# Performance work log

Hardware: AMD Instinct MI355X
Metric: run time of the kernel (lower is better)

The kernel has to match this reference:

```python
import jax, jax.numpy as jnp
import numpy as np

TAU = 0.2          # rank_temperature
LAM = 8.0          # lambda_value
TOPO = 0.5         # topology_influence
LEN_C = 0.01       # edge_length_coeff
SP_C = 0.001       # edge_sparsity_coeff
B, M, D = 4096, 256, 256


def _pairwise_sq(a, b):
    # [Na, D] x [Nb, D] -> [Na, Nb] squared L2 distances
    sq = (jnp.sum(a * a, -1)[:, None] - 2.0 * (a @ b.T)
          + jnp.sum(b * b, -1)[None, :])
    return jnp.maximum(sq, 0.0)


def setup_inputs() -> dict:
    key = jax.random.key(0)
    k1, k2, k3 = jax.random.split(key, 3)
    data = jax.random.normal(k1, (B, D), dtype=jnp.float32)
    weights = jax.random.uniform(k2, (M, D), dtype=jnp.float32)
    # edge logits initialized near edge_init_logit (-2.0) with small noise
    edge_logits = -2.0 + 0.1 * jax.random.normal(k3, (M, M), dtype=jnp.float32)
    return {"data": data, "weights": weights, "edge_logits": edge_logits}


def reference(data, weights, edge_logits):
    m = weights.shape[0]
    eye = jnp.eye(m, dtype=data.dtype)

    # distances: [B, M], l2
    distances = jnp.sqrt(_pairwise_sq(data, weights))

    # soft rank: [B, M]; pairwise sigmoid with zeroed diagonal
    diff = (distances[:, :, None] - distances[:, None, :]) / TAU  # [B, M, M]
    prob_greater = jax.nn.sigmoid(diff) * (1.0 - eye)[None]
    soft_rank = 1.0 + jnp.sum(prob_greater, axis=-1)

    # exponential neighborhood weighting
    neighborhood = jnp.exp(-(soft_rank - 1.0) / LAM)

    # symmetric edge probabilities with zero diagonal
    logits = 0.5 * (edge_logits + edge_logits.T)
    edge_prob = jax.nn.sigmoid(logits) * (1.0 - eye)

    degree = jnp.sum(edge_prob, axis=1) / float(m - 1)
    neighborhood = neighborhood * (1.0 + TOPO * degree[None, :])

    data_term = jnp.mean(neighborhood * distances)

    proto_dist = _pairwise_sq(weights, weights)  # sq_l2
    weighted_len = jnp.sum(edge_prob * proto_dist) / (jnp.sum(edge_prob) + 1e-8)
    sparsity = jnp.mean(edge_prob)

    loss = data_term + LEN_C * weighted_len + SP_C * sparsity
    return loss
```

## Files before the change

### kernel.cpp

```cpp
#include <hip/hip_runtime.h>
#include <math.h>

#define B_N 4096
#define M_N 256
#define D_N 256
#define ROWS 4
#define GRID_MAIN (B_N / ROWS)
#define NSLOT 64
#define BLK_PER_SLOT (GRID_MAIN / NSLOT)

constexpr float TAU_   = 0.2f;
constexpr float LAM_   = 8.0f;
constexpr float TOPO_  = 0.5f;
constexpr float LEN_C_ = 0.01f;
constexpr float SP_C_  = 0.001f;
constexpr float LOG2E_ = 1.44269504088896340736f;
constexpr float KSC    = LOG2E_ / TAU_;
constexpr float KL     = LOG2E_ / LAM_;
constexpr float C0_    = 133.0f;


__device__ __forceinline__ float wave_reduce_sum(float v) {
#pragma unroll
  for (int off = 1; off < 64; off <<= 1) v += __shfl_xor(v, off, 64);
  return v;
}

__global__ __launch_bounds__(256) void k_prep(const float* __restrict__ w,
                                              const float* __restrict__ E,
                                              float* __restrict__ ws) {
  int tid = threadIdx.x;
  if (blockIdx.x < M_N) {
    float* wT = ws + 8192;
    int j = blockIdx.x, d = tid;
    float v = w[j * D_N + d];
    wT[d * M_N + j] = v;
    float s = wave_reduce_sum(v * v);
    __shared__ float red[4];
    if ((d & 63) == 0) red[d >> 6] = s;
    if (j == 0) {
      if (d < 16) ws[d] = 0.0f;
      if (d < NSLOT) {
        ws[2048 + 16 * d] = 0.0f;
        ((unsigned*)ws)[4096 + 16 * d] = 0u;
      }
    }
    __syncthreads();
    if (d == 0) ws[512 + j] = red[0] + red[1] + red[2] + red[3];
  } else {
    int j = blockIdx.x - M_N;
    int k = tid;
    __shared__ __align__(16) float swj[D_N];
    __shared__ float redp[4], redw[4];
    swj[k] = w[j * D_N + k];
    __syncthreads();

    float l = 0.5f * (E[j * M_N + k] + E[k * M_N + j]);
    float p = __builtin_amdgcn_rcpf(1.0f + __builtin_amdgcn_exp2f(-l * LOG2E_));
    if (k == j) p = 0.0f;

    float pd = 0.0f;
    const float4* wr = (const float4*)(w + (size_t)k * D_N);
    const float4* sw = (const float4*)swj;
#pragma unroll 8
    for (int i = 0; i < D_N / 4; i++) {
      float4 a = wr[i], b = sw[i];
      float dx = a.x - b.x, dy = a.y - b.y, dz = a.z - b.z, dw = a.w - b.w;
      pd += dx * dx + dy * dy + dz * dz + dw * dw;
    }

    float sp  = wave_reduce_sum(p);
    float spd = wave_reduce_sum(p * pd);
    if ((k & 63) == 0) { redp[k >> 6] = sp; redw[k >> 6] = spd; }
    __syncthreads();
    if (k == 0) {
      float tp = redp[0] + redp[1] + redp[2] + redp[3];
      float tw = redw[0] + redw[1] + redw[2] + redw[3];
      ws[16 + j]   = tp * (1.0f / (float)(M_N - 1));
      ws[1024 + j] = tp;
      ws[1280 + j] = tw;
    }
  }
}

__global__ __launch_bounds__(256) void k_main(const float* __restrict__ data,
                                              float* __restrict__ ws,
                                              float* __restrict__ out) {
  const float* wT     = ws + 8192;
  const float* wnorm  = ws + 512;
  const float* degree = ws + 16;
  float* S_slot  = ws + 2048;
  unsigned* cnt1 = (unsigned*)ws + 4096;
  unsigned* cnt2 = (unsigned*)ws + 4;

  __shared__ __align__(16) float ew[ROWS][M_N];
  __shared__ __align__(16) float ewp[ROWS][M_N];
  __shared__ float rednrm[ROWS][4];
  __shared__ float snrm[ROWS];
  __shared__ float redf[4], redp[4], redw[4];
  __shared__ int isLast;

  const int tid  = threadIdx.x;
  const int wv_  = tid >> 6;
  const int lane = tid & 63;
  const int b0   = blockIdx.x * ROWS;

#pragma unroll
  for (int r = 0; r < ROWS; r++) {
    float x = data[(size_t)(b0 + r) * D_N + tid];
    float s = wave_reduce_sum(x * x);
    if (lane == 0) rednrm[r][wv_] = s;
  }
  __syncthreads();
  if (tid < ROWS)
    snrm[tid] = rednrm[tid][0] + rednrm[tid][1] + rednrm[tid][2] + rednrm[tid][3];

  const float4* x0 = (const float4*)(data + (size_t)(b0 + 0) * D_N);
  const float4* x1 = (const float4*)(data + (size_t)(b0 + 1) * D_N);
  const float4* x2 = (const float4*)(data + (size_t)(b0 + 2) * D_N);
  const float4* x3 = (const float4*)(data + (size_t)(b0 + 3) * D_N);
  float a0 = 0.f, a1 = 0.f, a2 = 0.f, a3 = 0.f;
#pragma unroll 4
  for (int d4 = 0; d4 < D_N / 4; d4++) {
    float4 xa = x0[d4], xb = x1[d4], xc = x2[d4], xd = x3[d4];
    const float* p = wT + (size_t)(4 * d4) * M_N + tid;
    float w0 = p[0], w1 = p[M_N], w2 = p[2 * M_N], w3 = p[3 * M_N];
    a0 = fmaf(xa.x, w0, a0); a0 = fmaf(xa.y, w1, a0);
    a0 = fmaf(xa.z, w2, a0); a0 = fmaf(xa.w, w3, a0);
    a1 = fmaf(xb.x, w0, a1); a1 = fmaf(xb.y, w1, a1);
    a1 = fmaf(xb.z, w2, a1); a1 = fmaf(xb.w, w3, a1);
    a2 = fmaf(xc.x, w0, a2); a2 = fmaf(xc.y, w1, a2);
    a2 = fmaf(xc.z, w2, a2); a2 = fmaf(xc.w, w3, a2);
    a3 = fmaf(xd.x, w0, a3); a3 = fmaf(xd.y, w1, a3);
    a3 = fmaf(xd.z, w2, a3); a3 = fmaf(xd.w, w3, a3);
  }
  __syncthreads();

  float wn = wnorm[tid];
  float acc[ROWS] = {a0, a1, a2, a3};
  float dist[ROWS], iv[ROWS], iv2[ROWS];
#pragma unroll
  for (int r = 0; r < ROWS; r++) {
    float sq = snrm[r] - 2.0f * acc[r] + wn;
    dist[r] = sqrtf(fmaxf(sq, 0.0f));
    float sc = dist[r] * KSC;
    ew[r][tid] = __builtin_amdgcn_exp2f(sc - C0_);
    iv[r]      = __builtin_amdgcn_exp2f(C0_ - sc);
    iv2[r]     = iv[r] * iv[r];
  }
  __syncthreads();

#pragma unroll
  for (int h = 0; h < 2; h++) {
    int p  = tid + h * 256;
    int r  = p >> 7, idx = p & 127;
    float ea = ew[r][2 * idx], eb = ew[r][2 * idx + 1];
    ewp[r][2 * idx]     = ea + eb;
    ewp[r][2 * idx + 1] = ea * eb;
  }
  __syncthreads();

  float fj = 1.0f + TOPO_ * degree[tid];
  float tl = 0.0f;
#pragma unroll
  for (int r = 0; r < ROWS; r++) {
    float s = 0.0f;
    const float4* q4 = (const float4*)(&ewp[r][0]);
    float ivr = iv[r], iv2r = iv2[r];
#pragma unroll 8
    for (int k4 = 0; k4 < M_N / 4; k4++) {
      float4 q = q4[k4];
      float t1 = ivr * q.x;
      s = fmaf(t1 + 2.0f, __builtin_amdgcn_rcpf(fmaf(iv2r, q.y, t1 + 1.0f)), s);
      float t2 = ivr * q.z;
      s = fmaf(t2 + 2.0f, __builtin_amdgcn_rcpf(fmaf(iv2r, q.w, t2 + 1.0f)), s);
    }
    float nb = __builtin_amdgcn_exp2f((0.5f - s) * KL);
    tl = fmaf(nb * dist[r], fj, tl);
  }

  float bs = wave_reduce_sum(tl);
  if (lane == 0) redf[wv_] = bs;
  __syncthreads();
  if (tid == 0) {
    float tot = redf[0] + redf[1] + redf[2] + redf[3];
    int slot = (int)(blockIdx.x & (NSLOT - 1));
    float old = atomicAdd(&S_slot[16 * slot], tot);
    asm volatile("" : "+v"(old));
    int last = 0;
    unsigned t1 = atomicAdd(&cnt1[16 * slot], 1u);
    if (t1 == (unsigned)(BLK_PER_SLOT - 1)) {
      unsigned t2 = atomicAdd(cnt2, 1u);
      last = (t2 == (unsigned)(NSLOT - 1)) ? 1 : 0;
    }
    isLast = last;
  }
  __syncthreads();

  if (isLast) {
    float p  = ws[1024 + tid];
    float wd = ws[1280 + tid];
    float rp = wave_reduce_sum(p);
    float rw = wave_reduce_sum(wd);
    if (lane == 0) { redp[wv_] = rp; redw[wv_] = rw; }
    float sd = 0.0f;
    if (wv_ == 0) {
      float v = atomicAdd(&S_slot[16 * lane], 0.0f);
      sd = wave_reduce_sum(v);
    }
    __syncthreads();
    if (tid == 0) {
      float Sp   = redp[0] + redp[1] + redp[2] + redp[3];
      float Swpd = redw[0] + redw[1] + redw[2] + redw[3];
      float data_term = sd * (1.0f / ((float)B_N * (float)M_N));
      float wl = Swpd / (Sp + 1e-8f);
      float sparsity = Sp * (1.0f / ((float)M_N * (float)M_N));
      out[0] = data_term + LEN_C_ * wl + SP_C_ * sparsity;
    }
  }
}

extern "C" void kernel_launch(void* const* d_in, const int* in_sizes, int n_in,
                              void* d_out, int out_size, void* d_ws, size_t ws_size,
                              hipStream_t stream) {
  const float* data = (const float*)d_in[0];
  const float* w    = (const float*)d_in[1];
  const float* E    = (const float*)d_in[2];
  float* ws = (float*)d_ws;

  k_prep<<<2 * M_N, 256, 0, stream>>>(w, E, ws);
  k_main<<<GRID_MAIN, 256, 0, stream>>>(data, ws, (float*)d_out);
}
```

Before: 102.2 us.

## Overlap soft-rank of rows 0-1 with distance matmul of rows 2-3

Splits the per-block work into two halves: the dot products for the first two data rows are computed first, and then their soft-rank pairwise loop is interleaved with the weight loads and FMAs for the remaining two rows. The aim is to hide global/L2 latency of the wT and data loads behind the transcendental-heavy rank computation instead of running the two phases back to back. In exchange it adds extra barriers and a second ewp build pass, raises register pressure from the 16-entry weight buffer, and re-reads wT per row pair.

New measurement: 114.5 us. +12.1%, slower.

```diff
diff --git a/kernel.cpp b/kernel.cpp
--- a/kernel.cpp
+++ b/kernel.cpp
@@ -24,6 +24,12 @@
 #pragma unroll
   for (int off = 1; off < 64; off <<= 1) v += __shfl_xor(v, off, 64);
   return v;
+}
+
+__device__ __forceinline__ void rank_pair(float iv, float iv2, float es,
+                                          float ep, float& s) {
+  float t = iv * es;
+  s = fmaf(t + 2.0f, __builtin_amdgcn_rcpf(fmaf(iv2, ep, t + 1.0f)), s);
 }
 
 __global__ __launch_bounds__(256) void k_prep(const float* __restrict__ w,
@@ -119,29 +125,26 @@
   const float4* x1 = (const float4*)(data + (size_t)(b0 + 1) * D_N);
   const float4* x2 = (const float4*)(data + (size_t)(b0 + 2) * D_N);
   const float4* x3 = (const float4*)(data + (size_t)(b0 + 3) * D_N);
-  float a0 = 0.f, a1 = 0.f, a2 = 0.f, a3 = 0.f;
-#pragma unroll 4
+
+  float a0 = 0.f, a1 = 0.f;
+#pragma unroll 8
   for (int d4 = 0; d4 < D_N / 4; d4++) {
-    float4 xa = x0[d4], xb = x1[d4], xc = x2[d4], xd = x3[d4];
     const float* p = wT + (size_t)(4 * d4) * M_N + tid;
     float w0 = p[0], w1 = p[M_N], w2 = p[2 * M_N], w3 = p[3 * M_N];
+    float4 xa = x0[d4], xb = x1[d4];
     a0 = fmaf(xa.x, w0, a0); a0 = fmaf(xa.y, w1, a0);
     a0 = fmaf(xa.z, w2, a0); a0 = fmaf(xa.w, w3, a0);
     a1 = fmaf(xb.x, w0, a1); a1 = fmaf(xb.y, w1, a1);
     a1 = fmaf(xb.z, w2, a1); a1 = fmaf(xb.w, w3, a1);
-    a2 = fmaf(xc.x, w0, a2); a2 = fmaf(xc.y, w1, a2);
-    a2 = fmaf(xc.z, w2, a2); a2 = fmaf(xc.w, w3, a2);
-    a3 = fmaf(xd.x, w0, a3); a3 = fmaf(xd.y, w1, a3);
-    a3 = fmaf(xd.z, w2, a3); a3 = fmaf(xd.w, w3, a3);
   }
   __syncthreads();
 
   float wn = wnorm[tid];
-  float acc[ROWS] = {a0, a1, a2, a3};
   float dist[ROWS], iv[ROWS], iv2[ROWS];
 #pragma unroll
-  for (int r = 0; r < ROWS; r++) {
-    float sq = snrm[r] - 2.0f * acc[r] + wn;
+  for (int r = 0; r < 2; r++) {
+    float a = (r == 0) ? a0 : a1;
+    float sq = snrm[r] - 2.0f * a + wn;
     dist[r] = sqrtf(fmaxf(sq, 0.0f));
     float sc = dist[r] * KSC;
     ew[r][tid] = __builtin_amdgcn_exp2f(sc - C0_);
@@ -150,32 +153,89 @@
   }
   __syncthreads();
 
-#pragma unroll
-  for (int h = 0; h < 2; h++) {
-    int p  = tid + h * 256;
-    int r  = p >> 7, idx = p & 127;
+  {
+    int r = tid >> 7, idx = tid & 127;
     float ea = ew[r][2 * idx], eb = ew[r][2 * idx + 1];
     ewp[r][2 * idx]     = ea + eb;
     ewp[r][2 * idx + 1] = ea * eb;
   }
   __syncthreads();
 
+  float a2 = 0.f, a3 = 0.f;
+  float s0 = 0.f, s1 = 0.f;
+  const float4* q0 = (const float4*)(&ewp[0][0]);
+  const float4* q1 = (const float4*)(&ewp[1][0]);
+  float iv0 = iv[0], iv20 = iv2[0], iv1 = iv[1], iv21 = iv2[1];
+#pragma unroll 2
+  for (int g = 0; g < 16; g++) {
+    float wreg[16];
+    const float* p = wT + (size_t)(16 * g) * M_N + tid;
+#pragma unroll
+    for (int i = 0; i < 16; i++) wreg[i] = p[(size_t)i * M_N];
+#pragma unroll
+    for (int k4 = 4 * g; k4 < 4 * g + 4; k4++) {
+      float4 qa = q0[k4];
+      rank_pair(iv0, iv20, qa.x, qa.y, s0);
+      rank_pair(iv0, iv20, qa.z, qa.w, s0);
+      float4 qb = q1[k4];
+      rank_pair(iv1, iv21, qb.x, qb.y, s1);
+      rank_pair(iv1, iv21, qb.z, qb.w, s1);
+    }
+#pragma unroll
+    for (int i4 = 0; i4 < 4; i4++) {
+      float4 xc = x2[4 * g + i4];
+      float4 xd = x3[4 * g + i4];
+      a2 = fmaf(xc.x, wreg[4 * i4 + 0], a2);
+      a2 = fmaf(xc.y, wreg[4 * i4 + 1], a2);
+      a2 = fmaf(xc.z, wreg[4 * i4 + 2], a2);
+      a2 = fmaf(xc.w, wreg[4 * i4 + 3], a2);
+      a3 = fmaf(xd.x, wreg[4 * i4 + 0], a3);
+      a3 = fmaf(xd.y, wreg[4 * i4 + 1], a3);
+      a3 = fmaf(xd.z, wreg[4 * i4 + 2], a3);
+      a3 = fmaf(xd.w, wreg[4 * i4 + 3], a3);
+    }
+  }
+
+#pragma unroll
+  for (int r = 2; r < 4; r++) {
+    float a = (r == 2) ? a2 : a3;
+    float sq = snrm[r] - 2.0f * a + wn;
+    dist[r] = sqrtf(fmaxf(sq, 0.0f));
+    float sc = dist[r] * KSC;
+    ew[r][tid] = __builtin_amdgcn_exp2f(sc - C0_);
+    iv[r]      = __builtin_amdgcn_exp2f(C0_ - sc);
+    iv2[r]     = iv[r] * iv[r];
+  }
+  __syncthreads();
+
+  {
+    int r = 2 + (tid >> 7), idx = tid & 127;
+    float ea = ew[r][2 * idx], eb = ew[r][2 * idx + 1];
+    ewp[r][2 * idx]     = ea + eb;
+    ewp[r][2 * idx + 1] = ea * eb;
+  }
+  __syncthreads();
+
+  float s2 = 0.f, s3 = 0.f;
+  const float4* q2 = (const float4*)(&ewp[2][0]);
+  const float4* q3 = (const float4*)(&ewp[3][0]);
+  float iv_2 = iv[2], iv22 = iv2[2], iv_3 = iv[3], iv23 = iv2[3];
+#pragma unroll 8
+  for (int k4 = 0; k4 < M_N / 4; k4++) {
+    float4 qa = q2[k4];
+    rank_pair(iv_2, iv22, qa.x, qa.y, s2);
+    rank_pair(iv_2, iv22, qa.z, qa.w, s2);
+    float4 qb = q3[k4];
+    rank_pair(iv_3, iv23, qb.x, qb.y, s3);
+    rank_pair(iv_3, iv23, qb.z, qb.w, s3);
+  }
+
   float fj = 1.0f + TOPO_ * degree[tid];
+  float ssum[ROWS] = {s0, s1, s2, s3};
   float tl = 0.0f;
 #pragma unroll
   for (int r = 0; r < ROWS; r++) {
-    float s = 0.0f;
-    const float4* q4 = (const float4*)(&ewp[r][0]);
-    float ivr = iv[r], iv2r = iv2[r];
-#pragma unroll 8
-    for (int k4 = 0; k4 < M_N / 4; k4++) {
-      float4 q = q4[k4];
-      float t1 = ivr * q.x;
-      s = fmaf(t1 + 2.0f, __builtin_amdgcn_rcpf(fmaf(iv2r, q.y, t1 + 1.0f)), s);
-      float t2 = ivr * q.z;
-      s = fmaf(t2 + 2.0f, __builtin_amdgcn_rcpf(fmaf(iv2r, q.w, t2 + 1.0f)), s);
-    }
-    float nb = __builtin_amdgcn_exp2f((0.5f - s) * KL);
+    float nb = __builtin_amdgcn_exp2f((0.5f - ssum[r]) * KL);
     tl = fmaf(nb * dist[r], fj, tl);
   }
 
```
